# Kernel optimization log

Hardware: AMD Instinct MI355X
Metric: run time of the kernel (lower is better)

## Reference

```python
import jax, jax.numpy as jnp
import numpy as np

HEAD_SIZE = 64
N_EMBD = 1024
B, T = 8, 2048


def setup_inputs() -> dict:
    key = jax.random.key(0)
    kx, kk, kq, kv = jax.random.split(key, 4)
    scale = 1.0 / np.sqrt(N_EMBD)
    return {
        "x": jax.random.normal(kx, (B, T, N_EMBD), dtype=jnp.float32),
        "Wk": jax.random.normal(kk, (N_EMBD, HEAD_SIZE), dtype=jnp.float32) * scale,
        "Wq": jax.random.normal(kq, (N_EMBD, HEAD_SIZE), dtype=jnp.float32) * scale,
        "Wv": jax.random.normal(kv, (N_EMBD, HEAD_SIZE), dtype=jnp.float32) * scale,
    }


def reference(x, Wk, Wq, Wv):
    # x: [B, T, E]; W*: [E, H] (equivalent to x @ nn.Linear.weight.T)
    k = jnp.einsum("bte,eh->bth", x, Wk)
    q = jnp.einsum("bte,eh->bth", x, Wq)
    v = jnp.einsum("bte,eh->bth", x, Wv)
    head_size = k.shape[-1]
    # scores: [B, T, T]
    wei = jnp.einsum("bqh,bkh->bqk", q, k) * (head_size ** -0.5)
    t = x.shape[1]
    causal = jnp.tril(jnp.ones((t, t), dtype=bool))  # [T, T]
    wei = jnp.where(causal, wei, -jnp.inf)
    wei = jax.nn.softmax(wei, axis=-1)
    # dropout p=0.0 -> identity
    out = jnp.einsum("bqk,bkh->bqh", wei, v)
    return out
```

## Files before the change

kernel.cpp:

```cpp
#include <hip/hip_runtime.h>
#include <cstdint>

#define BATCH 8
#define T_SEQ 2048
#define E_DIM 1024
#define H_DIM 64
#define BT (BATCH * T_SEQ)

typedef __attribute__((ext_vector_type(8))) short bf16x8;
typedef __attribute__((ext_vector_type(4))) float f32x4;

static __device__ __forceinline__ short f2bf(float f) {
    uint32_t b = __float_as_uint(f);
    b += 0x7fffu + ((b >> 16) & 1u);
    return (short)(b >> 16);
}

static __device__ __forceinline__ bf16x8 cvt8f(f32x4 a, f32x4 b) {
    union { bf16x8 v; uint32_t u[4]; } r;
    asm("v_cvt_pk_bf16_f32 %0, %1, %2" : "=v"(r.u[0]) : "v"(a.x), "v"(a.y));
    asm("v_cvt_pk_bf16_f32 %0, %1, %2" : "=v"(r.u[1]) : "v"(a.z), "v"(a.w));
    asm("v_cvt_pk_bf16_f32 %0, %1, %2" : "=v"(r.u[2]) : "v"(b.x), "v"(b.y));
    asm("v_cvt_pk_bf16_f32 %0, %1, %2" : "=v"(r.u[3]) : "v"(b.z), "v"(b.w));
    return r.v;
}

#define Q_OFF   0
#define K_OFF   (BT * H_DIM)
#define VT_OFF  (2 * BT * H_DIM)
#define WT_OFF  (3 * BT * H_DIM)

static __device__ __forceinline__ void glds16(const void* g, void* l) {
    __builtin_amdgcn_global_load_lds(
        (const __attribute__((address_space(1))) void*)g,
        (__attribute__((address_space(3))) void*)l, 16, 0, 0);
}


__global__ void wt_prep_frag(const float* __restrict__ Wk, const float* __restrict__ Wq,
                             const float* __restrict__ Wv, short* __restrict__ wtb) {
    int gid = blockIdx.x * 256 + threadIdx.x;
    int lane = gid & 63;
    int kt = (gid >> 6) & 31;
    int f = gid >> 11;
    int m = f >> 2, ct = f & 3;
    int col = (ct << 4) | (lane & 15);
    int k0 = (kt << 5) | (((lane >> 4) & 3) << 3);
    const float* W = (m == 0) ? Wk : ((m == 1) ? Wq : Wv);
    bf16x8 v;
    #pragma unroll
    for (int e = 0; e < 8; ++e) v[e] = f2bf(W[(size_t)(k0 + e) * H_DIM + col]);
    *reinterpret_cast<bf16x8*>(wtb + (size_t)gid * 8) = v;
}

__global__ __launch_bounds__(256, 2) void proj7(
    const float* __restrict__ x, const short* __restrict__ wtb,
    short* __restrict__ qo, short* __restrict__ kb_, short* __restrict__ vb_)
{
    __shared__ __align__(16) short Bs[2][24 * 512];
    __shared__ __align__(16) float Xs[2][2048];

    const int tid  = threadIdx.x;
    const int lane = tid & 63;
    const int w    = tid >> 6;
    const int kh   = w >> 1;
    const int rtl  = w & 1;
    const int rt_g = blockIdx.x * 2 + rtl;
    const int row0 = blockIdx.x * 32;

    const f32x4 z4 = {0.f, 0.f, 0.f, 0.f};
    f32x4 acc[12];
    #pragma unroll
    for (int f = 0; f < 12; ++f) acc[f] = z4;

    #define STAGE(dbuf, ss)                                                              \
        {                                                                                \
            _Pragma("unroll")                                                            \
            for (int ci = 0; ci < 6; ++ci) {                                             \
                int c = w * 6 + ci;                                                      \
                int f = c % 12, khc = c / 12;                                            \
                const short* src = wtb + (((size_t)f * 32 + khc * 16 + (ss)) * 64 + lane) * 8; \
                glds16(src, &Bs[dbuf][c * 512]);                                         \
            }                                                                            \
            _Pragma("unroll")                                                            \
            for (int i = 0; i < 2; ++i) {                                                \
                int ch = w * 2 + i;                                                      \
                int slc = ch >> 2, cc = ch & 3;                                          \
                const float* srcA = x + (size_t)(row0 + cc * 8 + (lane >> 3)) * E_DIM    \
                                      + slc * 512 + (ss) * 32                            \
                                      + (((lane & 7) ^ (lane >> 3)) << 2);               \
                glds16(srcA, &Xs[dbuf][ch * 256]);                                       \
            }                                                                            \
        }

    STAGE(0, 0);

    const int r8  = lane & 7;
    const int j0  = (lane >> 4) << 1;
    const int chA = (kh << 2) | (rtl << 1) | ((lane >> 3) & 1);
    const int g0  = r8 * 8 + (j0 ^ r8);
    const int g1  = r8 * 8 + ((j0 + 1) ^ r8);

    int buf = 0;
    for (int s = 0; s < 16; ++s) {
        if (s < 15) {
            STAGE(buf ^ 1, s + 1);
            asm volatile("s_waitcnt vmcnt(8)" ::: "memory");
        } else {
            asm volatile("s_waitcnt vmcnt(0)" ::: "memory");
        }
        __builtin_amdgcn_s_barrier();

        f32x4 a = *reinterpret_cast<const f32x4*>(&Xs[buf][chA * 256 + g0 * 4]);
        f32x4 b = *reinterpret_cast<const f32x4*>(&Xs[buf][chA * 256 + g1 * 4]);
        bf16x8 afc = cvt8f(a, b);
        #pragma unroll
        for (int f = 0; f < 12; ++f) {
            bf16x8 bfv = *reinterpret_cast<const bf16x8*>(&Bs[buf][(kh * 12 + f) * 512 + lane * 8]);
            acc[f] = __builtin_amdgcn_mfma_f32_16x16x32_bf16(afc, bfv, acc[f], 0, 0, 0);
        }
        __builtin_amdgcn_s_barrier();
        buf ^= 1;
    }

    float* mrg = reinterpret_cast<float*>(&Bs[0][0]);
    if (kh == 1) {
        #pragma unroll
        for (int f = 0; f < 12; ++f)
            *reinterpret_cast<f32x4*>(mrg + ((size_t)(rtl * 12 + f) * 64 + lane) * 4) = acc[f];
    }
    __syncthreads();
    if (kh == 0) {
        const int col16 = lane & 15, rowb = (lane >> 4) << 2;
        const int R0 = rt_g * 16 + rowb;
        #pragma unroll
        for (int m = 0; m < 3; ++m) {
            #pragma unroll
            for (int ct = 0; ct < 4; ++ct) {
                int f = m * 4 + ct;
                f32x4 v = acc[f];
                f32x4 o = *reinterpret_cast<const f32x4*>(mrg + ((size_t)(rtl * 12 + f) * 64 + lane) * 4);
                v.x += o.x; v.y += o.y; v.z += o.z; v.w += o.w;
                int C = (ct << 4) | col16;
                #pragma unroll
                for (int i = 0; i < 4; ++i) {
                    int R = R0 + i;
                    int b = R >> 11, tok = R & 2047, tt = tok >> 6;
                    if (m == 1) {
                        qo[(size_t)R * H_DIM + C] = f2bf(v[i] * 0.125f);
                    } else if (m == 0) {
                        int ctk = (tok >> 4) & 3, lnk = (tok & 15) | (((C >> 3) & 3) << 4);
                        int sk = C >> 5, ek = C & 7;
                        kb_[(((((size_t)b * 32 + tt) * 4 + ctk) * 2 + sk) * 64 + lnk) * 8 + ek] = f2bf(v[i]);
                    } else {
                        int sv = (tok >> 5) & 1, gv = (tok >> 3) & 3, ev = tok & 7;
                        int dtv = C >> 4, lnv = (C & 15) | (gv << 4);
                        vb_[(((((size_t)b * 32 + tt) * 4 + dtv) * 2 + sv) * 64 + lnv) * 8 + ev] = f2bf(v[i]);
                    }
                }
            }
        }
    }
}

#define SWZ(row, off) ((off) ^ (((row) & 7) << 3))

__global__ __launch_bounds__(512, 4) void attn3(
    const short* __restrict__ q, const short* __restrict__ kb,
    const short* __restrict__ vb, float* __restrict__ out)
{
    __shared__ __align__(16) short Ps[8][16 * 64];
    __shared__ float Og[4][16][64];
    __shared__ float Mg[4][16], Lg[4][16];

    const int tid  = threadIdx.x;
    const int lane = tid & 63;
    const int w    = tid >> 6;
    const int band = w & 1;
    const int kq   = w >> 1;
    const int bb   = blockIdx.x & 7;
    const int j    = blockIdx.x >> 3;
    const int p    = (j < 32) ? (63 - j) : (j - 32);

    const int q0 = p << 5;
    const int Nt = (p >> 1) + 1;

    const int qrowA = q0 + (band << 4) + (lane & 15);
    bf16x8 qf[2];
    #pragma unroll
    for (int s = 0; s < 2; ++s)
        qf[s] = *reinterpret_cast<const bf16x8*>(
            q + (size_t)(bb * T_SEQ + qrowA) * H_DIM + s * 32 + ((lane >> 4) << 3));

    const f32x4 z4 = {0.f, 0.f, 0.f, 0.f};
    float mreg[4] = {-1e30f, -1e30f, -1e30f, -1e30f};
    float lreg[4] = {0.f, 0.f, 0.f, 0.f};
    f32x4 oacc[4] = {z4, z4, z4, z4};

    const short* kbb = kb + (size_t)bb * 32 * 4096;
    const short* vbb = vb + (size_t)bb * 32 * 4096;

    for (int t = kq; t < Nt; t += 4) {
        const short* kt = kbb + (size_t)t * 4096 + lane * 8;
        f32x4 sacc[4] = {z4, z4, z4, z4};
        #pragma unroll
        for (int s = 0; s < 2; ++s)
            #pragma unroll
            for (int ct = 0; ct < 4; ++ct) {
                bf16x8 bfv = *reinterpret_cast<const bf16x8*>(kt + (ct * 2 + s) * 512);
                sacc[ct] = __builtin_amdgcn_mfma_f32_16x16x32_bf16(qf[s], bfv, sacc[ct], 0, 0, 0);
            }
        const short* vt_ = vbb + (size_t)t * 4096 + lane * 8;
        bf16x8 Vc[8];
        #pragma unroll
        for (int u = 0; u < 8; ++u)
            Vc[u] = *reinterpret_cast<const bf16x8*>(vt_ + u * 512);
        if (t == Nt - 1) {
            int qgb = q0 + (band << 4) + ((lane >> 4) << 2);
            #pragma unroll
            for (int ct = 0; ct < 4; ++ct) {
                int kg = t * 64 + (ct << 4) + (lane & 15);
                #pragma unroll
                for (int i = 0; i < 4; ++i)
                    if (kg > qgb + i) sacc[ct][i] = -1e30f;
            }
        }
        #pragma unroll
        for (int i = 0; i < 4; ++i) {
            float s0 = sacc[0][i], s1 = sacc[1][i], s2 = sacc[2][i], s3 = sacc[3][i];
            float tmax = fmaxf(fmaxf(s0, s1), fmaxf(s2, s3));
            tmax = fmaxf(tmax, __shfl_xor(tmax, 1));
            tmax = fmaxf(tmax, __shfl_xor(tmax, 2));
            tmax = fmaxf(tmax, __shfl_xor(tmax, 4));
            tmax = fmaxf(tmax, __shfl_xor(tmax, 8));
            float mnew = fmaxf(mreg[i], tmax);
            float sc = __expf(mreg[i] - mnew);
            mreg[i] = mnew;
            float p0 = __expf(s0 - mnew), p1 = __expf(s1 - mnew);
            float p2 = __expf(s2 - mnew), p3 = __expf(s3 - mnew);
            float ps = p0 + p1 + p2 + p3;
            ps += __shfl_xor(ps, 1); ps += __shfl_xor(ps, 2);
            ps += __shfl_xor(ps, 4); ps += __shfl_xor(ps, 8);
            lreg[i] = lreg[i] * sc + ps;
            oacc[0][i] *= sc; oacc[1][i] *= sc; oacc[2][i] *= sc; oacc[3][i] *= sc;
            int rq = ((lane >> 4) << 2) + i;
            short* pr = &Ps[w][rq * 64];
            pr[SWZ(rq, (0 << 4) + (lane & 15))] = f2bf(p0);
            pr[SWZ(rq, (1 << 4) + (lane & 15))] = f2bf(p1);
            pr[SWZ(rq, (2 << 4) + (lane & 15))] = f2bf(p2);
            pr[SWZ(rq, (3 << 4) + (lane & 15))] = f2bf(p3);
        }
        int qa = lane & 15;
        #pragma unroll
        for (int dt = 0; dt < 4; ++dt)
            #pragma unroll
            for (int s = 0; s < 2; ++s) {
                int koff = s * 32 + ((lane >> 4) << 3);
                bf16x8 af = *reinterpret_cast<const bf16x8*>(&Ps[w][qa * 64 + SWZ(qa, koff)]);
                oacc[dt] = __builtin_amdgcn_mfma_f32_16x16x32_bf16(af, Vc[dt * 2 + s], oacc[dt], 0, 0, 0);
            }
    }

    __syncthreads();
    if (kq >= 2) {
        int slot = (band << 1) | (kq - 2);
        #pragma unroll
        for (int i = 0; i < 4; ++i) {
            int rq = ((lane >> 4) << 2) + i;
            #pragma unroll
            for (int dt = 0; dt < 4; ++dt)
                Og[slot][rq][(dt << 4) + (lane & 15)] = oacc[dt][i];
            if ((lane & 15) == 0) { Mg[slot][rq] = mreg[i]; Lg[slot][rq] = lreg[i]; }
        }
    }
    __syncthreads();
    if (kq < 2) {
        int slot = (band << 1) | kq;
        #pragma unroll
        for (int i = 0; i < 4; ++i) {
            int rq = ((lane >> 4) << 2) + i;
            float m1 = Mg[slot][rq], l1 = Lg[slot][rq];
            float mm = fmaxf(mreg[i], m1);
            float f0 = __expf(mreg[i] - mm), f1 = __expf(m1 - mm);
            mreg[i] = mm;
            lreg[i] = lreg[i] * f0 + l1 * f1;
            #pragma unroll
            for (int dt = 0; dt < 4; ++dt)
                oacc[dt][i] = oacc[dt][i] * f0 + Og[slot][rq][(dt << 4) + (lane & 15)] * f1;
        }
    }
    __syncthreads();
    if (kq == 1) {
        int slot = (band << 1) | 1;
        #pragma unroll
        for (int i = 0; i < 4; ++i) {
            int rq = ((lane >> 4) << 2) + i;
            #pragma unroll
            for (int dt = 0; dt < 4; ++dt)
                Og[slot][rq][(dt << 4) + (lane & 15)] = oacc[dt][i];
            if ((lane & 15) == 0) { Mg[slot][rq] = mreg[i]; Lg[slot][rq] = lreg[i]; }
        }
    }
    __syncthreads();
    if (kq == 0) {
        int slot = (band << 1) | 1;
        #pragma unroll
        for (int i = 0; i < 4; ++i) {
            int rq = ((lane >> 4) << 2) + i;
            float m1 = Mg[slot][rq], l1 = Lg[slot][rq];
            float mm = fmaxf(mreg[i], m1);
            float f0 = __expf(mreg[i] - mm), f1 = __expf(m1 - mm);
            float l  = lreg[i] * f0 + l1 * f1;
            float inv = 1.f / l;
            size_t orow = (size_t)(bb * T_SEQ + q0 + (band << 4) + rq) * H_DIM;
            #pragma unroll
            for (int dt = 0; dt < 4; ++dt) {
                float ov = oacc[dt][i] * f0 + Og[slot][rq][(dt << 4) + (lane & 15)] * f1;
                out[orow + (dt << 4) + (lane & 15)] = ov * inv;
            }
        }
    }
}

extern "C" void kernel_launch(void* const* d_in, const int* in_sizes, int n_in,
                              void* d_out, int out_size, void* d_ws, size_t ws_size,
                              hipStream_t stream) {
    const float* x  = (const float*)d_in[0];
    const float* Wk = (const float*)d_in[1];
    const float* Wq = (const float*)d_in[2];
    const float* Wv = (const float*)d_in[3];
    float* out = (float*)d_out;

    short* ws  = (short*)d_ws;
    short* qb  = ws + Q_OFF;
    short* kbp = ws + K_OFF;
    short* vbp = ws + VT_OFF;
    short* wtb = ws + WT_OFF;

    wt_prep_frag<<<96, 256, 0, stream>>>(Wk, Wq, Wv, wtb);
    proj7<<<BT / 32, 256, 0, stream>>>(x, wtb, qb, kbp, vbp);
    attn3<<<512, 512, 0, stream>>>(qb, kbp, vbp, out);
}
```

Baseline: 45.57 us.

## Split attention work by 32-key half-tiles across 8 waves, each covering all 32 query rows

Reorganises the attention kernel so each of the 8 waves processes both 16-row query bands against 32-key half-tiles, in place of the old layout of 2 bands × 4 key-groups over 64-key tiles. This balances causal work more finely across waves and reuses each loaded K/V fragment for two query bands, halving per-wave K/V global loads per key. In exchange, the cross-wave softmax merge grows to a 3-level tree reduction over 32 rows with more barriers and shared-memory traffic, and register pressure rises from doubled accumulators.

```diff
diff --git a/kernel.cpp b/kernel.cpp
--- a/kernel.cpp
+++ b/kernel.cpp
@@ -163,162 +163,171 @@
     }
 }
 
-#define SWZ(row, off) ((off) ^ (((row) & 7) << 3))
-
-__global__ __launch_bounds__(512, 4) void attn3(
+__global__ __launch_bounds__(512, 4) void attn8(
     const short* __restrict__ q, const short* __restrict__ kb,
     const short* __restrict__ vb, float* __restrict__ out)
 {
-    __shared__ __align__(16) short Ps[8][16 * 64];
-    __shared__ float Og[4][16][64];
-    __shared__ float Mg[4][16], Lg[4][16];
+    __shared__ __align__(16) short Ps[8 * 1024];
+    __shared__ float Og[4][32][64];
+    __shared__ float Mg[4][32], Lg[4][32];
 
     const int tid  = threadIdx.x;
     const int lane = tid & 63;
     const int w    = tid >> 6;
-    const int band = w & 1;
-    const int kq   = w >> 1;
+    const int l15  = lane & 15;
+    const int l4   = lane >> 4;
     const int bb   = blockIdx.x & 7;
     const int j    = blockIdx.x >> 3;
     const int p    = (j < 32) ? (63 - j) : (j - 32);
 
     const int q0 = p << 5;
-    const int Nt = (p >> 1) + 1;
-
-    const int qrowA = q0 + (band << 4) + (lane & 15);
-    bf16x8 qf[2];
+
+    bf16x8 qf[2][2];
     #pragma unroll
-    for (int s = 0; s < 2; ++s)
-        qf[s] = *reinterpret_cast<const bf16x8*>(
-            q + (size_t)(bb * T_SEQ + qrowA) * H_DIM + s * 32 + ((lane >> 4) << 3));
+    for (int qe = 0; qe < 2; ++qe)
+        #pragma unroll
+        for (int s = 0; s < 2; ++s)
+            qf[qe][s] = *reinterpret_cast<const bf16x8*>(
+                q + (size_t)(bb * T_SEQ + q0 + qe * 16 + l15) * H_DIM + s * 32 + l4 * 8);
 
     const f32x4 z4 = {0.f, 0.f, 0.f, 0.f};
-    float mreg[4] = {-1e30f, -1e30f, -1e30f, -1e30f};
-    float lreg[4] = {0.f, 0.f, 0.f, 0.f};
-    f32x4 oacc[4] = {z4, z4, z4, z4};
+    float mreg[2][4], lreg[2][4];
+    f32x4 oacc[2][4];
+    #pragma unroll
+    for (int qe = 0; qe < 2; ++qe)
+        #pragma unroll
+        for (int i = 0; i < 4; ++i) {
+            mreg[qe][i] = -1e30f; lreg[qe][i] = 0.f; oacc[qe][i] = z4;
+        }
 
     const short* kbb = kb + (size_t)bb * 32 * 4096;
     const short* vbb = vb + (size_t)bb * 32 * 4096;
-
-    for (int t = kq; t < Nt; t += 4) {
-        const short* kt = kbb + (size_t)t * 4096 + lane * 8;
-        f32x4 sacc[4] = {z4, z4, z4, z4};
-        #pragma unroll
-        for (int s = 0; s < 2; ++s)
-            #pragma unroll
-            for (int ct = 0; ct < 4; ++ct) {
-                bf16x8 bfv = *reinterpret_cast<const bf16x8*>(kt + (ct * 2 + s) * 512);
-                sacc[ct] = __builtin_amdgcn_mfma_f32_16x16x32_bf16(qf[s], bfv, sacc[ct], 0, 0, 0);
+    short* psw = &Ps[w * 1024];
+
+    for (int g = w; g <= p; g += 8) {
+        const int t = g >> 1, h = g & 1;
+        const short* kt = kbb + (size_t)t * 4096 + h * 2048 + lane * 8;
+        const short* vt = vbb + (size_t)t * 4096 + h * 512 + lane * 8;
+        bf16x8 Kc[4];
+        #pragma unroll
+        for (int cth = 0; cth < 2; ++cth)
+            #pragma unroll
+            for (int s = 0; s < 2; ++s)
+                Kc[cth * 2 + s] = *reinterpret_cast<const bf16x8*>(kt + cth * 1024 + s * 512);
+        f32x4 sacc[2][2] = {{z4, z4}, {z4, z4}};
+        #pragma unroll
+        for (int qe = 0; qe < 2; ++qe)
+            #pragma unroll
+            for (int cth = 0; cth < 2; ++cth) {
+                sacc[qe][cth] = __builtin_amdgcn_mfma_f32_16x16x32_bf16(qf[qe][0], Kc[cth * 2 + 0], sacc[qe][cth], 0, 0, 0);
+                sacc[qe][cth] = __builtin_amdgcn_mfma_f32_16x16x32_bf16(qf[qe][1], Kc[cth * 2 + 1], sacc[qe][cth], 0, 0, 0);
             }
-        const short* vt_ = vbb + (size_t)t * 4096 + lane * 8;
-        bf16x8 Vc[8];
-        #pragma unroll
-        for (int u = 0; u < 8; ++u)
-            Vc[u] = *reinterpret_cast<const bf16x8*>(vt_ + u * 512);
-        if (t == Nt - 1) {
-            int qgb = q0 + (band << 4) + ((lane >> 4) << 2);
-            #pragma unroll
-            for (int ct = 0; ct < 4; ++ct) {
-                int kg = t * 64 + (ct << 4) + (lane & 15);
+        bf16x8 Vc[4];
+        #pragma unroll
+        for (int dt = 0; dt < 4; ++dt)
+            Vc[dt] = *reinterpret_cast<const bf16x8*>(vt + dt * 1024);
+        if (g == p) {
+            #pragma unroll
+            for (int qe = 0; qe < 2; ++qe)
                 #pragma unroll
-                for (int i = 0; i < 4; ++i)
-                    if (kg > qgb + i) sacc[ct][i] = -1e30f;
+                for (int cth = 0; cth < 2; ++cth) {
+                    int kgl = cth * 16 + l15;
+                    #pragma unroll
+                    for (int i = 0; i < 4; ++i)
+                        if (kgl > qe * 16 + l4 * 4 + i) sacc[qe][cth][i] = -1e30f;
+                }
+        }
+        #pragma unroll
+        for (int qe = 0; qe < 2; ++qe)
+            #pragma unroll
+            for (int i = 0; i < 4; ++i) {
+                float s0 = sacc[qe][0][i], s1 = sacc[qe][1][i];
+                float tmax = fmaxf(s0, s1);
+                tmax = fmaxf(tmax, __shfl_xor(tmax, 1));
+                tmax = fmaxf(tmax, __shfl_xor(tmax, 2));
+                tmax = fmaxf(tmax, __shfl_xor(tmax, 4));
+                tmax = fmaxf(tmax, __shfl_xor(tmax, 8));
+                float mnew = fmaxf(mreg[qe][i], tmax);
+                float sc = __expf(mreg[qe][i] - mnew);
+                mreg[qe][i] = mnew;
+                float p0 = __expf(s0 - mnew), p1 = __expf(s1 - mnew);
+                float ps = p0 + p1;
+                ps += __shfl_xor(ps, 1); ps += __shfl_xor(ps, 2);
+                ps += __shfl_xor(ps, 4); ps += __shfl_xor(ps, 8);
+                lreg[qe][i] = lreg[qe][i] * sc + ps;
+                #pragma unroll
+                for (int dt = 0; dt < 4; ++dt) oacc[qe][dt][i] *= sc;
+                int row = qe * 16 + l4 * 4 + i;
+                int rs = (row >> 1) & 3;
+                psw[row * 32 + (((l15 >> 3) ^ rs)) * 8 + (l15 & 7)]       = f2bf(p0);
+                psw[row * 32 + (((2 + (l15 >> 3)) ^ rs)) * 8 + (l15 & 7)] = f2bf(p1);
             }
-        }
-        #pragma unroll
-        for (int i = 0; i < 4; ++i) {
-            float s0 = sacc[0][i], s1 = sacc[1][i], s2 = sacc[2][i], s3 = sacc[3][i];
-            float tmax = fmaxf(fmaxf(s0, s1), fmaxf(s2, s3));
-            tmax = fmaxf(tmax, __shfl_xor(tmax, 1));
-            tmax = fmaxf(tmax, __shfl_xor(tmax, 2));
-            tmax = fmaxf(tmax, __shfl_xor(tmax, 4));
-            tmax = fmaxf(tmax, __shfl_xor(tmax, 8));
-            float mnew = fmaxf(mreg[i], tmax);
-            float sc = __expf(mreg[i] - mnew);
-            mreg[i] = mnew;
-            float p0 = __expf(s0 - mnew), p1 = __expf(s1 - mnew);
-            float p2 = __expf(s2 - mnew), p3 = __expf(s3 - mnew);
-            float ps = p0 + p1 + p2 + p3;
-            ps += __shfl_xor(ps, 1); ps += __shfl_xor(ps, 2);
-            ps += __shfl_xor(ps, 4); ps += __shfl_xor(ps, 8);
-            lreg[i] = lreg[i] * sc + ps;
-            oacc[0][i] *= sc; oacc[1][i] *= sc; oacc[2][i] *= sc; oacc[3][i] *= sc;
-            int rq = ((lane >> 4) << 2) + i;
-            short* pr = &Ps[w][rq * 64];
-            pr[SWZ(rq, (0 << 4) + (lane & 15))] = f2bf(p0);
-            pr[SWZ(rq, (1 << 4) + (lane & 15))] = f2bf(p1);
-            pr[SWZ(rq, (2 << 4) + (lane & 15))] = f2bf(p2);
-            pr[SWZ(rq, (3 << 4) + (lane & 15))] = f2bf(p3);
-        }
-        int qa = lane & 15;
-        #pragma unroll
-        for (int dt = 0; dt < 4; ++dt)
-            #pragma unroll
-            for (int s = 0; s < 2; ++s) {
-                int koff = s * 32 + ((lane >> 4) << 3);
-                bf16x8 af = *reinterpret_cast<const bf16x8*>(&Ps[w][qa * 64 + SWZ(qa, koff)]);
-                oacc[dt] = __builtin_amdgcn_mfma_f32_16x16x32_bf16(af, Vc[dt * 2 + s], oacc[dt], 0, 0, 0);
+        #pragma unroll
+        for (int qe = 0; qe < 2; ++qe) {
+            int row = qe * 16 + l15;
+            bf16x8 af = *reinterpret_cast<const bf16x8*>(
+                &psw[row * 32 + ((l4 ^ ((row >> 1) & 3))) * 8]);
+            #pragma unroll
+            for (int dt = 0; dt < 4; ++dt)
+                oacc[qe][dt] = __builtin_amdgcn_mfma_f32_16x16x32_bf16(af, Vc[dt], oacc[qe][dt], 0, 0, 0);
+        }
+    }
+
+    #define DUMP(slot)                                                                 \
+        {                                                                              \
+            _Pragma("unroll")                                                          \
+            for (int qe = 0; qe < 2; ++qe)                                             \
+                _Pragma("unroll")                                                      \
+                for (int i = 0; i < 4; ++i) {                                          \
+                    int row = qe * 16 + l4 * 4 + i;                                    \
+                    _Pragma("unroll")                                                  \
+                    for (int dt = 0; dt < 4; ++dt)                                     \
+                        Og[slot][row][dt * 16 + l15] = oacc[qe][dt][i];                \
+                    if (l15 == 0) { Mg[slot][row] = mreg[qe][i]; Lg[slot][row] = lreg[qe][i]; } \
+                }                                                                      \
+        }
+    #define MERGE(slot)                                                                \
+        {                                                                              \
+            _Pragma("unroll")                                                          \
+            for (int qe = 0; qe < 2; ++qe)                                             \
+                _Pragma("unroll")                                                      \
+                for (int i = 0; i < 4; ++i) {                                          \
+                    int row = qe * 16 + l4 * 4 + i;                                    \
+                    float m1 = Mg[slot][row], l1 = Lg[slot][row];                      \
+                    float mm = fmaxf(mreg[qe][i], m1);                                 \
+                    float f0 = __expf(mreg[qe][i] - mm), f1 = __expf(m1 - mm);         \
+                    mreg[qe][i] = mm;                                                  \
+                    lreg[qe][i] = lreg[qe][i] * f0 + l1 * f1;                          \
+                    _Pragma("unroll")                                                  \
+                    for (int dt = 0; dt < 4; ++dt)                                     \
+                        oacc[qe][dt][i] = oacc[qe][dt][i] * f0 + Og[slot][row][dt * 16 + l15] * f1; \
+                }                                                                      \
+        }
+
+    __syncthreads();
+    if (w >= 4) DUMP(w - 4);
+    __syncthreads();
+    if (w < 4) MERGE(w);
+    __syncthreads();
+    if (w == 2 || w == 3) DUMP(w - 2);
+    __syncthreads();
+    if (w < 2) MERGE(w);
+    __syncthreads();
+    if (w == 1) DUMP(0);
+    __syncthreads();
+    if (w == 0) {
+        MERGE(0);
+        #pragma unroll
+        for (int qe = 0; qe < 2; ++qe)
+            #pragma unroll
+            for (int i = 0; i < 4; ++i) {
+                int row = qe * 16 + l4 * 4 + i;
+                float inv = 1.f / lreg[qe][i];
+                size_t orow = (size_t)(bb * T_SEQ + q0 + row) * H_DIM;
+                #pragma unroll
+                for (int dt = 0; dt < 4; ++dt)
+                    out[orow + dt * 16 + l15] = oacc[qe][dt][i] * inv;
             }
-    }
-
-    __syncthreads();
-    if (kq >= 2) {
-        int slot = (band << 1) | (kq - 2);
-        #pragma unroll
-        for (int i = 0; i < 4; ++i) {
-            int rq = ((lane >> 4) << 2) + i;
-            #pragma unroll
-            for (int dt = 0; dt < 4; ++dt)
-                Og[slot][rq][(dt << 4) + (lane & 15)] = oacc[dt][i];
-            if ((lane & 15) == 0) { Mg[slot][rq] = mreg[i]; Lg[slot][rq] = lreg[i]; }
-        }
-    }
-    __syncthreads();
-    if (kq < 2) {
-        int slot = (band << 1) | kq;
-        #pragma unroll
-        for (int i = 0; i < 4; ++i) {
-            int rq = ((lane >> 4) << 2) + i;
-            float m1 = Mg[slot][rq], l1 = Lg[slot][rq];
-            float mm = fmaxf(mreg[i], m1);
-            float f0 = __expf(mreg[i] - mm), f1 = __expf(m1 - mm);
-            mreg[i] = mm;
-            lreg[i] = lreg[i] * f0 + l1 * f1;
-            #pragma unroll
-            for (int dt = 0; dt < 4; ++dt)
-                oacc[dt][i] = oacc[dt][i] * f0 + Og[slot][rq][(dt << 4) + (lane & 15)] * f1;
-        }
-    }
-    __syncthreads();
-    if (kq == 1) {
-        int slot = (band << 1) | 1;
-        #pragma unroll
-        for (int i = 0; i < 4; ++i) {
-            int rq = ((lane >> 4) << 2) + i;
-            #pragma unroll
-            for (int dt = 0; dt < 4; ++dt)
-                Og[slot][rq][(dt << 4) + (lane & 15)] = oacc[dt][i];
-            if ((lane & 15) == 0) { Mg[slot][rq] = mreg[i]; Lg[slot][rq] = lreg[i]; }
-        }
-    }
-    __syncthreads();
-    if (kq == 0) {
-        int slot = (band << 1) | 1;
-        #pragma unroll
-        for (int i = 0; i < 4; ++i) {
-            int rq = ((lane >> 4) << 2) + i;
-            float m1 = Mg[slot][rq], l1 = Lg[slot][rq];
-            float mm = fmaxf(mreg[i], m1);
-            float f0 = __expf(mreg[i] - mm), f1 = __expf(m1 - mm);
-            float l  = lreg[i] * f0 + l1 * f1;
-            float inv = 1.f / l;
-            size_t orow = (size_t)(bb * T_SEQ + q0 + (band << 4) + rq) * H_DIM;
-            #pragma unroll
-            for (int dt = 0; dt < 4; ++dt) {
-                float ov = oacc[dt][i] * f0 + Og[slot][rq][(dt << 4) + (lane & 15)] * f1;
-                out[orow + (dt << 4) + (lane & 15)] = ov * inv;
-            }
-        }
     }
 }
 
@@ -339,5 +348,5 @@
 
     wt_prep_frag<<<96, 256, 0, stream>>>(Wk, Wq, Wv, wtb);
     proj7<<<BT / 32, 256, 0, stream>>>(x, wtb, qb, kbp, vbp);
-    attn3<<<512, 512, 0, stream>>>(qb, kbp, vbp, out);
-}
+    attn8<<<512, 512, 0, stream>>>(qb, kbp, vbp, out);
+}
```

Result: slower. 57.74 us (+26.7%).
